# Kernel optimization log

Hardware: AMD Instinct MI355X
Metric: run time of the kernel (lower is better)

Reference implementation:

```python
import jax, jax.numpy as jnp
import numpy as np

B, N, D, DC, R = 32, 36, 2048, 4, 512  # batch, regions, feat dim, coord dim, fusion rank


def setup_inputs() -> dict:
    key = jax.random.key(0)
    ks = jax.random.split(key, 8)
    s = lambda fan_in: 1.0 / np.sqrt(fan_in)
    return {
        "mm": jax.random.normal(ks[0], (B, N, D), dtype=jnp.float32),
        "coords": jax.random.uniform(ks[1], (B, N, DC), dtype=jnp.float32),
        "U_feat": jax.random.normal(ks[2], (D, R), dtype=jnp.float32) * s(D),
        "V_feat": jax.random.normal(ks[3], (D, R), dtype=jnp.float32) * s(D),
        "P_feat": jax.random.normal(ks[4], (R, D), dtype=jnp.float32) * s(R),
        "U_coord": jax.random.normal(ks[5], (DC, R), dtype=jnp.float32) * s(DC),
        "V_coord": jax.random.normal(ks[6], (DC, R), dtype=jnp.float32) * s(DC),
        "P_coord": jax.random.normal(ks[7], (R, D), dtype=jnp.float32) * s(R),
    }


def reference(mm, coords, U_feat, V_feat, P_feat, U_coord, V_coord, P_coord):
    # Pairwise module: build all (i, j) region pairs, fuse, max-aggregate over j.
    # Original torch code detach_()'s the gathered pair tensors -> stop_gradient here.
    mm_sg = jax.lax.stop_gradient(mm)
    coords_sg = jax.lax.stop_gradient(coords)

    # Coord fusion (MLB-style low-rank multiplicative fusion)
    uc = jnp.einsum("bnc,cr->bnr", coords_sg, U_coord)   # [B,N,R]
    vc = jnp.einsum("bnc,cr->bnr", coords_sg, V_coord)   # [B,N,R]
    zc = jax.nn.relu(uc[:, :, None, :] * vc[:, None, :, :])  # [B,N,N,R]
    Rij = jnp.einsum("bijr,rd->bijd", zc, P_coord)       # [B,N,N,D]

    # Feature fusion
    uf = jnp.einsum("bnd,dr->bnr", mm_sg, U_feat)
    vf = jnp.einsum("bnd,dr->bnr", mm_sg, V_feat)
    zf = jax.nn.relu(uf[:, :, None, :] * vf[:, None, :, :])  # [B,N,N,R]
    Rij = Rij + jnp.einsum("bijr,rd->bijd", zf, P_feat)  # [B,N,N,D]

    # agg['type'] == 'max': reduce over the second region axis (j)
    mm_new = jnp.max(Rij, axis=2)                        # [B,N,D]

    # residual
    return mm_new + mm
```

## Files before the change

### kernel.cpp

```cpp
#include <hip/hip_runtime.h>

#define BI    1152
#define NREG  36
#define DD    2048
#define RR    512
#define KK    1024
#define ZROWS (BI*NREG)
#define MBLK  144
#define NBLK  256
#define ABUF  (MBLK*32)
#define BBUF  (NBLK*32)
#define BUFE  (ABUF+BBUF)

typedef __bf16 bf16;
typedef __bf16 bf16x8 __attribute__((ext_vector_type(8)));
typedef __bf16 bf16x4 __attribute__((ext_vector_type(4)));
typedef float  f32x4  __attribute__((ext_vector_type(4)));

__device__ __forceinline__ void gl_lds16(const void* g, void* l) {
  __builtin_amdgcn_global_load_lds(
      (const __attribute__((address_space(1))) unsigned int*)g,
      (__attribute__((address_space(3))) unsigned int*)l, 16, 0, 0);
}

__global__ void k_prep(const float* __restrict__ mm, const float* __restrict__ coords,
                       const float* __restrict__ U_feat, const float* __restrict__ V_feat,
                       const float* __restrict__ P_feat, const float* __restrict__ U_coord,
                       const float* __restrict__ V_coord, const float* __restrict__ P_coord,
                       bf16* __restrict__ mmb, bf16* __restrict__ UT, bf16* __restrict__ VT,
                       bf16* __restrict__ PTt, float* __restrict__ uc, float* __restrict__ vc) {
  __shared__ float tile[32][33];
  int bid = blockIdx.x, tid = threadIdx.x;
  if (bid < 2304) {
    int i = bid * 256 + tid;
    float4 v = ((const float4*)mm)[i];
    bf16x4 o = {(bf16)v.x, (bf16)v.y, (bf16)v.z, (bf16)v.w};
    ((bf16x4*)mmb)[i] = o;
  } else if (bid < 4352) {
    int rel = bid - 2304;
    int zz = rel >> 10, rr = rel & 1023;
    int c0 = (rr & 15) * 32, r0 = (rr >> 4) * 32;
    const float* in = zz ? V_feat : U_feat;
    bf16* outp = zz ? VT : UT;
    int tx = tid & 31, ty = tid >> 5;
#pragma unroll
    for (int k = 0; k < 4; k++)
      tile[ty + 8 * k][tx] = in[(long)(r0 + ty + 8 * k) * 512 + c0 + tx];
    __syncthreads();
#pragma unroll
    for (int k = 0; k < 4; k++)
      outp[(long)(c0 + ty + 8 * k) * 2048 + r0 + tx] = (bf16)tile[tx][ty + 8 * k];
  } else if (bid < 6400) {
    int rel = bid - 4352;
    int zz = rel >> 10, rr = rel & 1023;
    int c0 = (rr & 63) * 32, r0 = (rr >> 6) * 32;
    const float* in = zz ? P_feat : P_coord;
    int koff = zz * 512;
    int tx = tid & 31, ty = tid >> 5;
#pragma unroll
    for (int k = 0; k < 4; k++)
      tile[ty + 8 * k][tx] = in[(long)(r0 + ty + 8 * k) * 2048 + c0 + tx];
    __syncthreads();
    int kc = (koff + r0) >> 5;
#pragma unroll
    for (int k = 0; k < 4; k++) {
      int d = c0 + ty + 8 * k;
      PTt[((long)kc * 2048 + d) * 32 + tx] = (bf16)tile[tx][ty + 8 * k];
    }
  } else {
    int g = bid - 6400;
    float c0 = coords[g * 4 + 0], c1 = coords[g * 4 + 1];
    float c2 = coords[g * 4 + 2], c3 = coords[g * 4 + 3];
#pragma unroll
    for (int i = 0; i < 2; i++) {
      int r = tid + i * 256;
      uc[g * RR + r] = c0 * U_coord[r] + c1 * U_coord[RR + r] + c2 * U_coord[2 * RR + r] + c3 * U_coord[3 * RR + r];
      vc[g * RR + r] = c0 * V_coord[r] + c1 * V_coord[RR + r] + c2 * V_coord[2 * RR + r] + c3 * V_coord[3 * RR + r];
    }
  }
}

__launch_bounds__(256)
__global__ void k_gemm_uv(const bf16* __restrict__ mmb, const bf16* __restrict__ UT,
                          const bf16* __restrict__ VT, float* __restrict__ uf,
                          float* __restrict__ vf, float* __restrict__ uf2,
                          float* __restrict__ vf2) {
  __shared__ bf16 lds2[2][6144];
  int uv = blockIdx.z >> 1, kh = blockIdx.z & 1;
  const bf16* Bmat = uv ? VT : UT;
  float* outp = uv ? (kh ? vf2 : vf) : (kh ? uf2 : uf);
  int m0 = blockIdx.x * 64, n0 = blockIdx.y * 128;
  int kbase = kh * 1024;
  int tid = threadIdx.x, wave = tid >> 6, lane = tid & 63;
  int l15 = lane & 15, qv = lane >> 4;
  int qp_c = qv ^ ((l15 >> 1) & 3);
  int qs = (lane & 3) ^ ((lane >> 3) & 3);

  const bf16* gA = mmb + (long)(m0 + wave * 16 + (lane >> 2)) * 2048 + kbase + qs * 8;
  const bf16* gB = Bmat + (long)(n0 + wave * 32 + (lane >> 2)) * 2048 + kbase + qs * 8;
  int lA = wave * 512;
  int lB = 2048 + wave * 1024;

  auto stage = [&](int buf, int k0) {
    bf16* db = &lds2[buf][0];
    gl_lds16(gA + k0, db + lA);
    gl_lds16(gB + k0, db + lB);
    gl_lds16(gB + 16 * 2048 + k0, db + lB + 512);
  };

  f32x4 acc[4][2] = {};
  stage(0, 0);
  for (int k0 = 0; k0 < 1024; k0 += 32) {
    int cur = (k0 >> 5) & 1;
    __syncthreads();
    if (k0 + 32 < 1024) stage(cur ^ 1, k0 + 32);
    bf16x8 a[4], b[2];
#pragma unroll
    for (int mt = 0; mt < 4; mt++)
      a[mt] = *(const bf16x8*)(&lds2[cur][0] + (mt * 16 + l15) * 32 + qp_c * 8);
#pragma unroll
    for (int nt = 0; nt < 2; nt++)
      b[nt] = *(const bf16x8*)(&lds2[cur][2048] + (wave * 32 + nt * 16 + l15) * 32 + qp_c * 8);
#pragma unroll
    for (int mt = 0; mt < 4; mt++)
#pragma unroll
      for (int nt = 0; nt < 2; nt++)
        acc[mt][nt] = __builtin_amdgcn_mfma_f32_16x16x32_bf16(a[mt], b[nt], acc[mt][nt], 0, 0, 0);
  }
#pragma unroll
  for (int mt = 0; mt < 4; mt++)
#pragma unroll
    for (int nt = 0; nt < 2; nt++)
#pragma unroll
      for (int r = 0; r < 4; r++) {
        int row = m0 + mt * 16 + qv * 4 + r;
        int col = n0 + wave * 32 + nt * 16 + l15;
        outp[(long)row * RR + col] = acc[mt][nt][r];
      }
}

__global__ void k_build_z(const float* __restrict__ uc, const float* __restrict__ vc,
                          const float* __restrict__ uf, const float* __restrict__ vf,
                          const float* __restrict__ uf2, const float* __restrict__ vf2,
                          bf16* __restrict__ z) {
  __shared__ float uL[36 * 128];
  __shared__ float vL[36 * 128];
  int kq = blockIdx.x, b = blockIdx.y, tid = threadIdx.x;
  int kb = (kq & 3) * 128;
  for (int i = tid; i < 1152; i += 256) {
    int row = i >> 5, kk = (i & 31) * 4;
    long src = (long)(b * 36 + row) * RR + kb + kk;
    float4 u4, v4;
    if (kq < 4) {
      u4 = *(const float4*)(uc + src);
      v4 = *(const float4*)(vc + src);
    } else {
      float4 a1 = *(const float4*)(uf + src), a2 = *(const float4*)(uf2 + src);
      float4 b1 = *(const float4*)(vf + src), b2 = *(const float4*)(vf2 + src);
      u4.x = a1.x + a2.x; u4.y = a1.y + a2.y; u4.z = a1.z + a2.z; u4.w = a1.w + a2.w;
      v4.x = b1.x + b2.x; v4.y = b1.y + b2.y; v4.z = b1.z + b2.z; v4.w = b1.w + b2.w;
    }
    *(float4*)&uL[row * 128 + kk] = u4;
    *(float4*)&vL[row * 128 + kk] = v4;
  }
  __syncthreads();
  int cbase = blockIdx.z * 20736;
  for (int c = cbase + tid; c < cbase + 20736; c += 256) {
    int kcl = c / 10368;
    int rem = c - kcl * 10368;
    int row = rem >> 3;
    int x4 = rem & 7;
    int gl = row / 36;
    int j = row - gl * 36;
    int kl = kcl * 32 + x4 * 4;
    float4 u4 = *(const float4*)&uL[gl * 128 + kl];
    float4 v4 = *(const float4*)&vL[j * 128 + kl];
    float x0 = fmaxf(u4.x * v4.x, 0.f), x1 = fmaxf(u4.y * v4.y, 0.f);
    float x2 = fmaxf(u4.z * v4.z, 0.f), x3 = fmaxf(u4.w * v4.w, 0.f);
    bf16x4 o = {(bf16)x0, (bf16)x1, (bf16)x2, (bf16)x3};
    int bi = b * 36 + gl;
    long rowp = (long)(bi >> 2) * 144 + j * 4 + (bi & 3);
    *(bf16x4*)(z + ((long)(kq * 4 + kcl) * ZROWS + rowp) * 32 + x4 * 4) = o;
  }
}

__launch_bounds__(256, 2)
__global__ void k_main(const bf16* __restrict__ z, const bf16* __restrict__ PTt,
                       const float* __restrict__ mm, float* __restrict__ out) {
  __shared__ bf16 lds[2 * BUFE];
  int bid = blockIdx.x;
  int x = bid & 7, t = bid >> 3;
  int dt = t & 7, go = (t >> 3) * 8 + x;
  int d0 = dt * NBLK;
  int tid = threadIdx.x, wave = tid >> 6, lane = tid & 63;
  int l15 = lane & 15, qv = lane >> 4;
  int qp_c = qv ^ ((l15 >> 1) & 3);
  int qs = (lane & 3) ^ ((lane >> 3) & 3);
  int lroff = (lane >> 2) * 32 + qs * 8;

  const bf16* gA = z + (long)go * ABUF + wave * 1024 + lroff;
  const bf16* gB = PTt + (long)d0 * 32 + wave * 2048 + lroff;
  int lA = wave * 1024;
  int lB = ABUF + wave * 2048;

  int sbuf = 0;
  auto stage = [&]() {
    bf16* db = lds + sbuf * BUFE;
    gl_lds16(gA, db + lA);
    gl_lds16(gA + 512, db + lA + 512);
    if (wave == 0) gl_lds16(gA + 4096, db + 4096);
    gl_lds16(gB, db + lB);
    gl_lds16(gB + 512, db + lB + 512);
    gl_lds16(gB + 1024, db + lB + 1024);
    gl_lds16(gB + 1536, db + lB + 1536);
    gA += (long)ZROWS * 32;
    gB += 2048L * 32;
    sbuf ^= 1;
  };

  f32x4 acc[9][4] = {};
  stage();
  for (int kc = 0; kc < 32; kc++) {
    __syncthreads();
    if (kc < 31) stage();
    const bf16* cur = lds + (kc & 1) * BUFE;
    bf16x8 b[4];
#pragma unroll
    for (int nt = 0; nt < 4; nt++)
      b[nt] = *(const bf16x8*)(cur + ABUF + (wave * 64 + nt * 16 + l15) * 32 + qp_c * 8);
#pragma unroll
    for (int mt = 0; mt < 9; mt++) {
      bf16x8 av = *(const bf16x8*)(cur + (mt * 16 + l15) * 32 + qp_c * 8);
#pragma unroll
      for (int nt = 0; nt < 4; nt++)
        acc[mt][nt] = __builtin_amdgcn_mfma_f32_16x16x32_bf16(av, b[nt], acc[mt][nt], 0, 0, 0);
    }
  }

#pragma unroll
  for (int nt = 0; nt < 4; nt++) {
    float mx[4];
#pragma unroll
    for (int r = 0; r < 4; r++) {
      mx[r] = acc[0][nt][r];
#pragma unroll
      for (int mt = 1; mt < 9; mt++) mx[r] = fmaxf(mx[r], acc[mt][nt][r]);
      mx[r] = fmaxf(mx[r], __shfl_xor(mx[r], 16, 64));
      mx[r] = fmaxf(mx[r], __shfl_xor(mx[r], 32, 64));
    }
    if (lane < 16) {
      int col = d0 + wave * 64 + nt * 16 + lane;
#pragma unroll
      for (int r = 0; r < 4; r++) {
        long oa = (long)(go * 4 + r) * DD + col;
        out[oa] = mx[r] + mm[oa];
      }
    }
  }
}

extern "C" void kernel_launch(void* const* d_in, const int* in_sizes, int n_in,
                              void* d_out, int out_size, void* d_ws, size_t ws_size,
                              hipStream_t stream) {
  const float* mm     = (const float*)d_in[0];
  const float* coords = (const float*)d_in[1];
  const float* U_feat = (const float*)d_in[2];
  const float* V_feat = (const float*)d_in[3];
  const float* P_feat = (const float*)d_in[4];
  const float* U_coord= (const float*)d_in[5];
  const float* V_coord= (const float*)d_in[6];
  const float* P_coord= (const float*)d_in[7];
  float* out = (float*)d_out;

  char* ws = (char*)d_ws;
  bf16* z   = (bf16*)(ws + 0);
  bf16* PTt = (bf16*)(ws + 84934656);
  bf16* mmb = (bf16*)(ws + 89128960);
  bf16* UT  = (bf16*)(ws + 93847552);
  bf16* VT  = (bf16*)(ws + 95944704);
  float* uf = (float*)(ws + 98041856);
  float* vf = (float*)(ws + 100401152);
  float* uc = (float*)(ws + 102760448);
  float* vc = (float*)(ws + 105119744);
  float* uf2= (float*)(ws + 107479040);
  float* vf2= (float*)(ws + 109838336);

  k_prep<<<dim3(7552), dim3(256), 0, stream>>>(mm, coords, U_feat, V_feat, P_feat,
                                               U_coord, V_coord, P_coord,
                                               mmb, UT, VT, PTt, uc, vc);
  k_gemm_uv<<<dim3(18, 4, 4), dim3(256), 0, stream>>>(mmb, UT, VT, uf, vf, uf2, vf2);
  k_build_z<<<dim3(8, 32, 2), dim3(256), 0, stream>>>(uc, vc, uf, vf, uf2, vf2, z);
  k_main<<<dim3(2304), dim3(256), 0, stream>>>(z, PTt, mm, out);
}
```

Before: 249.5 us.

## Triple-buffer LDS staging with explicit vmcnt waits in main GEMM loop

The main loop now stages global-to-LDS loads three K-chunks ahead instead of one, using three LDS buffers. The single __syncthreads is replaced by per-wave s_waitcnt vmcnt counts, so each wave waits only for the oldest outstanding chunk, plus explicit barriers around the compute phase. The MFMA section is also raised to high wave priority with s_setprio. The goal is to hide more global load latency. The cost is 50% more LDS per block, which may hurt occupancy at two blocks per CU, and the hand-counted vmcnt values are fragile.

After: 255.1 us. +2.2%, slower.

```diff
diff --git a/kernel.cpp b/kernel.cpp
--- a/kernel.cpp
+++ b/kernel.cpp
@@ -187,7 +187,7 @@
 __launch_bounds__(256, 2)
 __global__ void k_main(const bf16* __restrict__ z, const bf16* __restrict__ PTt,
                        const float* __restrict__ mm, float* __restrict__ out) {
-  __shared__ bf16 lds[2 * BUFE];
+  __shared__ bf16 lds[3 * BUFE];
   int bid = blockIdx.x;
   int x = bid & 7, t = bid >> 3;
   int dt = t & 7, go = (t >> 3) * 8 + x;
@@ -203,9 +203,8 @@
   int lA = wave * 1024;
   int lB = ABUF + wave * 2048;
 
-  int sbuf = 0;
-  auto stage = [&]() {
-    bf16* db = lds + sbuf * BUFE;
+  auto stage = [&](int buf) {
+    bf16* db = lds + buf * BUFE;
     gl_lds16(gA, db + lA);
     gl_lds16(gA + 512, db + lA + 512);
     if (wave == 0) gl_lds16(gA + 4096, db + 4096);
@@ -215,19 +214,32 @@
     gl_lds16(gB + 1536, db + lB + 1536);
     gA += (long)ZROWS * 32;
     gB += 2048L * 32;
-    sbuf ^= 1;
   };
 
   f32x4 acc[9][4] = {};
-  stage();
+  stage(0);
+  stage(1);
+  stage(2);
+  int cb = 0;
   for (int kc = 0; kc < 32; kc++) {
-    __syncthreads();
-    if (kc < 31) stage();
-    const bf16* cur = lds + (kc & 1) * BUFE;
+    if (kc < 30) {
+      if (wave == 0) asm volatile("s_waitcnt vmcnt(14)" ::: "memory");
+      else           asm volatile("s_waitcnt vmcnt(12)" ::: "memory");
+    } else if (kc == 30) {
+      if (wave == 0) asm volatile("s_waitcnt vmcnt(7)" ::: "memory");
+      else           asm volatile("s_waitcnt vmcnt(6)" ::: "memory");
+    } else {
+      asm volatile("s_waitcnt vmcnt(0)" ::: "memory");
+    }
+    __builtin_amdgcn_s_barrier();
+    __builtin_amdgcn_sched_barrier(0);
+
+    const bf16* cur = lds + cb * BUFE;
     bf16x8 b[4];
 #pragma unroll
     for (int nt = 0; nt < 4; nt++)
       b[nt] = *(const bf16x8*)(cur + ABUF + (wave * 64 + nt * 16 + l15) * 32 + qp_c * 8);
+    __builtin_amdgcn_s_setprio(1);
 #pragma unroll
     for (int mt = 0; mt < 9; mt++) {
       bf16x8 av = *(const bf16x8*)(cur + (mt * 16 + l15) * 32 + qp_c * 8);
@@ -235,6 +247,12 @@
       for (int nt = 0; nt < 4; nt++)
         acc[mt][nt] = __builtin_amdgcn_mfma_f32_16x16x32_bf16(av, b[nt], acc[mt][nt], 0, 0, 0);
     }
+    __builtin_amdgcn_s_setprio(0);
+    asm volatile("s_waitcnt lgkmcnt(0)" ::: "memory");
+    __builtin_amdgcn_sched_barrier(0);
+    __builtin_amdgcn_s_barrier();
+    if (kc < 29) stage(cb);
+    cb = (cb == 2) ? 0 : cb + 1;
   }
 
 #pragma unroll
```

## Load B operand directly to registers and triple-buffer A in LDS

Applied to the files above, without the earlier changes.

The B tile (PTt) is no longer staged through LDS. Each lane loads its B fragments from global memory straight into registers, double-buffered across two register sets. The A tile moves to a three-stage LDS ring with explicit vmcnt waits, split barriers and raised wave priority around the MFMA block, so loads can run further ahead of compute. This removes B's LDS traffic and bank pressure but adds register pressure and relies on hand-counted vmcnt values that must match the issued loads exactly.

After: 259.0 us. 1.04x slower.

```diff
diff --git a/kernel.cpp b/kernel.cpp
--- a/kernel.cpp
+++ b/kernel.cpp
@@ -9,8 +9,6 @@
 #define MBLK  144
 #define NBLK  256
 #define ABUF  (MBLK*32)
-#define BBUF  (NBLK*32)
-#define BUFE  (ABUF+BBUF)
 
 typedef __bf16 bf16;
 typedef __bf16 bf16x8 __attribute__((ext_vector_type(8)));
@@ -187,7 +185,7 @@
 __launch_bounds__(256, 2)
 __global__ void k_main(const bf16* __restrict__ z, const bf16* __restrict__ PTt,
                        const float* __restrict__ mm, float* __restrict__ out) {
-  __shared__ bf16 lds[2 * BUFE];
+  __shared__ bf16 lds[3 * ABUF];
   int bid = blockIdx.x;
   int x = bid & 7, t = bid >> 3;
   int dt = t & 7, go = (t >> 3) * 8 + x;
@@ -199,43 +197,69 @@
   int lroff = (lane >> 2) * 32 + qs * 8;
 
   const bf16* gA = z + (long)go * ABUF + wave * 1024 + lroff;
-  const bf16* gB = PTt + (long)d0 * 32 + wave * 2048 + lroff;
   int lA = wave * 1024;
-  int lB = ABUF + wave * 2048;
-
-  int sbuf = 0;
-  auto stage = [&]() {
-    bf16* db = lds + sbuf * BUFE;
+  const bf16* gBr = PTt + (long)(d0 + wave * 64 + l15) * 32 + qv * 8;
+
+  auto stageA = [&](int buf) {
+    bf16* db = lds + buf * ABUF;
     gl_lds16(gA, db + lA);
     gl_lds16(gA + 512, db + lA + 512);
     if (wave == 0) gl_lds16(gA + 4096, db + 4096);
-    gl_lds16(gB, db + lB);
-    gl_lds16(gB + 512, db + lB + 512);
-    gl_lds16(gB + 1024, db + lB + 1024);
-    gl_lds16(gB + 1536, db + lB + 1536);
     gA += (long)ZROWS * 32;
-    gB += 2048L * 32;
-    sbuf ^= 1;
   };
 
+  bf16x8 pa[4], pb[4];
+  auto loadB = [&](int kcb, bf16x8 (&p)[4]) {
+#pragma unroll
+    for (int nt = 0; nt < 4; nt++)
+      p[nt] = *(const bf16x8*)(gBr + (long)kcb * 65536 + nt * 512);
+  };
+
   f32x4 acc[9][4] = {};
-  stage();
-  for (int kc = 0; kc < 32; kc++) {
-    __syncthreads();
-    if (kc < 31) stage();
-    const bf16* cur = lds + (kc & 1) * BUFE;
-    bf16x8 b[4];
-#pragma unroll
-    for (int nt = 0; nt < 4; nt++)
-      b[nt] = *(const bf16x8*)(cur + ABUF + (wave * 64 + nt * 16 + l15) * 32 + qp_c * 8);
-#pragma unroll
-    for (int mt = 0; mt < 9; mt++) {
-      bf16x8 av = *(const bf16x8*)(cur + (mt * 16 + l15) * 32 + qp_c * 8);
-#pragma unroll
-      for (int nt = 0; nt < 4; nt++)
-        acc[mt][nt] = __builtin_amdgcn_mfma_f32_16x16x32_bf16(av, b[nt], acc[mt][nt], 0, 0, 0);
-    }
-  }
+  stageA(0);
+  stageA(1);
+  loadB(0, pa);
+  stageA(2);
+  loadB(1, pb);
+  int cb = 0;
+
+#define KBODY(KC, PREG)                                                         \
+  {                                                                             \
+    int kc_ = (KC);                                                             \
+    if (kc_ < 30) {                                                             \
+      if (wave == 0) asm volatile("s_waitcnt vmcnt(7)" ::: "memory");           \
+      else           asm volatile("s_waitcnt vmcnt(6)" ::: "memory");           \
+    } else if (kc_ == 30) {                                                     \
+      asm volatile("s_waitcnt vmcnt(4)" ::: "memory");                          \
+    } else {                                                                    \
+      asm volatile("s_waitcnt vmcnt(0)" ::: "memory");                          \
+    }                                                                           \
+    __builtin_amdgcn_s_barrier();                                               \
+    __builtin_amdgcn_sched_barrier(0);                                          \
+    const bf16* cur = lds + cb * ABUF;                                          \
+    __builtin_amdgcn_s_setprio(1);                                              \
+    _Pragma("unroll")                                                           \
+    for (int mt = 0; mt < 9; mt++) {                                            \
+      bf16x8 av = *(const bf16x8*)(cur + (mt * 16 + l15) * 32 + qp_c * 8);      \
+      _Pragma("unroll")                                                         \
+      for (int nt = 0; nt < 4; nt++)                                            \
+        acc[mt][nt] = __builtin_amdgcn_mfma_f32_16x16x32_bf16(av, PREG[nt],     \
+                                                  acc[mt][nt], 0, 0, 0);        \
+    }                                                                           \
+    __builtin_amdgcn_s_setprio(0);                                              \
+    asm volatile("s_waitcnt lgkmcnt(0)" ::: "memory");                          \
+    __builtin_amdgcn_sched_barrier(0);                                          \
+    __builtin_amdgcn_s_barrier();                                               \
+    if (kc_ <= 28) stageA(cb);                                                  \
+    if (kc_ <= 29) loadB(kc_ + 2, PREG);                                        \
+    cb = (cb == 2) ? 0 : cb + 1;                                                \
+  }
+
+  for (int kc = 0; kc < 32; kc += 2) {
+    KBODY(kc, pa);
+    KBODY(kc + 1, pb);
+  }
+#undef KBODY
 
 #pragma unroll
   for (int nt = 0; nt < 4; nt++) {
```
